# Performance work log

Hardware: AMD Instinct MI355X
Metric: run time of the kernel (lower is better)

Reference implementation:

```python
import jax, jax.numpy as jnp
import numpy as np

B = 256          # batch
H = 1024         # conditioning_size (dec_hid_dim)
D = 256          # gst_dim
G = 32           # num_gst
C = 16           # num_cells
O = 256          # output_size


def setup_inputs() -> dict:
    key = jax.random.key(0)
    ks = jax.random.split(key, 7)
    hidden = jax.random.normal(ks[0], (B, H), dtype=jnp.float32)
    # per-cell embedding tables: nn.Embedding(num_gst, gst_dim) stacked over cells
    gst_emb = jax.random.normal(ks[1], (C, G, D), dtype=jnp.float32)
    # per-cell Linear(gst_dim + cond, cond): weight [H, H + D] (torch [out, in]), bias [H]
    attn_w = jax.random.normal(ks[2], (C, H, H + D), dtype=jnp.float32) * 0.02
    attn_b = jax.random.normal(ks[3], (C, H), dtype=jnp.float32) * 0.02
    # per-cell v: Parameter(torch.rand(cond))
    v = jax.random.uniform(ks[4], (C, H), dtype=jnp.float32)
    # out Linear(gst_dim, output_size)
    out_w = jax.random.normal(ks[5], (O, D), dtype=jnp.float32) * 0.02
    out_b = jax.random.normal(ks[6], (O,), dtype=jnp.float32) * 0.02
    return {"hidden": hidden, "gst_emb": gst_emb, "attn_w": attn_w,
            "attn_b": attn_b, "v": v, "out_w": out_w, "out_b": out_b}


def reference(hidden, gst_emb, attn_w, attn_b, v, out_w, out_b):
    # Original concatenates (hidden, encoder_outputs) along features; split the
    # linear weight accordingly instead of materializing the concat.
    w_hid = attn_w[:, :, :H]        # [C, H, H]
    w_enc = attn_w[:, :, H:]        # [C, H, D]
    # embedding lookup of arange(G) == the table rows themselves (same for all batch)
    enc = gst_emb                   # [C, G, D]
    hid_part = jnp.einsum('bh,coh->bco', hidden, w_hid)     # [B, C, Ho]
    enc_part = jnp.einsum('cgd,cod->cgo', enc, w_enc)       # [C, G, Ho]
    energy = jnp.tanh(hid_part[:, :, None, :] + enc_part[None]
                      + attn_b[None, :, None, :])           # [B, C, G, Ho]
    scores = jnp.einsum('bcgh,ch->bcg', energy, v)          # [B, C, G]
    attention = jax.nn.softmax(scores, axis=-1)             # softmax over num_gst
    weighted = jnp.einsum('bcg,cgd->bcd', attention, enc)   # [B, C, D]
    att_cat = attention.reshape(B, C * G)                   # torch.cat(att_list, dim=1)
    pooled = jnp.mean(weighted, axis=1)                     # [B, D]
    out = pooled @ out_w.T + out_b                          # [B, O]
    return (att_cat, out)
```

## Files before the change

### kernel.cpp

```cpp
#include <hip/hip_runtime.h>
#include <hip/hip_bf16.h>

#define B_  256
#define H_  1024
#define D_  256
#define G_  32
#define C_  16
#define O_  256
#define HD_ 1280
#define N1_ 16384
#define RS_ 36

typedef __attribute__((ext_vector_type(8))) short short8;
typedef __attribute__((ext_vector_type(4))) short s16x4;
typedef __attribute__((ext_vector_type(4))) float f32x4;

#define MFMA16(a, b, c) __builtin_amdgcn_mfma_f32_16x16x32_bf16((a), (b), (c), 0, 0, 0)

__device__ __forceinline__ float tanh_c(float x) {
    float y = __expf(2.f * x);
    float t = 1.f - 2.f * __builtin_amdgcn_rcpf(y + 1.f);
    return fminf(fmaxf(t, -0.99999994f), 0.99999994f);
}

__device__ __forceinline__ short bfhi(float x) {
    return (short)(__float_as_uint(x) >> 16);
}
__device__ __forceinline__ short bflo(float x) {
    float fhi = __uint_as_float(__float_as_uint(x) & 0xFFFF0000u);
    return (short)(__float_as_uint(x - fhi) >> 16);
}

__device__ __forceinline__ void split4(const float4 v, s16x4& hi, s16x4& lo) {
    hi[0] = bfhi(v.x); lo[0] = bflo(v.x);
    hi[1] = bfhi(v.y); lo[1] = bflo(v.y);
    hi[2] = bfhi(v.z); lo[2] = bflo(v.z);
    hi[3] = bfhi(v.w); lo[3] = bflo(v.w);
}

__global__ __launch_bounds__(256) void gemm12_kernel(
    const float* __restrict__ hidden, const float* __restrict__ enc,
    const float* __restrict__ attn_w, const float* __restrict__ attn_b,
    float* __restrict__ hp, float* __restrict__ ep)
{
    __shared__ short AsH[64 * RS_];
    __shared__ short AsL[64 * RS_];
    __shared__ short BsH[64 * RS_];
    __shared__ short BsL[64 * RS_];

    const int tid  = threadIdx.x;
    const int wave = tid >> 6, lane = tid & 63;
    const int l16 = lane & 15;
    const int lk  = (lane >> 4) * 8;

    if (blockIdx.x < 4) {
        const int m0 = blockIdx.x * 64;
        const int n0 = blockIdx.y * 64;
        const int wm = (wave >> 1) * 32;
        const int wn = (wave & 1) * 32;

        f32x4 acc[2][2];
        #pragma unroll
        for (int mi = 0; mi < 2; ++mi)
            #pragma unroll
            for (int ni = 0; ni < 2; ++ni)
                acc[mi][ni] = f32x4{0.f, 0.f, 0.f, 0.f};

        const int r0 = tid >> 3;
        const int c0 = (tid & 7) * 4;
        const float* pA = hidden + (size_t)(m0 + r0) * H_ + c0;
        const float* pB = attn_w + (size_t)(n0 + r0) * HD_ + c0;
        const int dA = 32 * H_;
        const int dB = 32 * HD_;

        float4 a0[2], a1[2], b0[2], b1[2];
        a0[0] = *(const float4*)(pA);
        a1[0] = *(const float4*)(pA + dA);
        b0[0] = *(const float4*)(pB);
        b1[0] = *(const float4*)(pB + dB);
        a0[1] = *(const float4*)(pA + 32);
        a1[1] = *(const float4*)(pA + dA + 32);
        b0[1] = *(const float4*)(pB + 32);
        b1[1] = *(const float4*)(pB + dB + 32);

#define G1_BODY(S, K0)                                                        \
        {                                                                     \
            __builtin_amdgcn_s_barrier();                                     \
            { s16x4 h_, l_; split4(a0[S], h_, l_);                            \
              *(s16x4*)(AsH + r0 * RS_ + c0) = h_;                            \
              *(s16x4*)(AsL + r0 * RS_ + c0) = l_; }                          \
            { s16x4 h_, l_; split4(a1[S], h_, l_);                            \
              *(s16x4*)(AsH + (r0 + 32) * RS_ + c0) = h_;                     \
              *(s16x4*)(AsL + (r0 + 32) * RS_ + c0) = l_; }                   \
            { s16x4 h_, l_; split4(b0[S], h_, l_);                            \
              *(s16x4*)(BsH + r0 * RS_ + c0) = h_;                            \
              *(s16x4*)(BsL + r0 * RS_ + c0) = l_; }                          \
            { s16x4 h_, l_; split4(b1[S], h_, l_);                            \
              *(s16x4*)(BsH + (r0 + 32) * RS_ + c0) = h_;                     \
              *(s16x4*)(BsL + (r0 + 32) * RS_ + c0) = l_; }                   \
            asm volatile("s_waitcnt lgkmcnt(0)" ::: "memory");                \
            __builtin_amdgcn_s_barrier();                                     \
            if ((K0) + 64 < H_) {                                             \
                a0[S] = *(const float4*)(pA + (K0) + 64);                     \
                a1[S] = *(const float4*)(pA + dA + (K0) + 64);                \
                b0[S] = *(const float4*)(pB + (K0) + 64);                     \
                b1[S] = *(const float4*)(pB + dB + (K0) + 64);                \
            }                                                                 \
            short8 ah_[2], al_[2], bh_[2], bl_[2];                            \
            _Pragma("unroll")                                                 \
            for (int mi = 0; mi < 2; ++mi) {                                  \
                ah_[mi] = *(const short8*)(AsH + (wm + mi * 16 + l16) * RS_ + lk); \
                al_[mi] = *(const short8*)(AsL + (wm + mi * 16 + l16) * RS_ + lk); \
            }                                                                 \
            _Pragma("unroll")                                                 \
            for (int ni = 0; ni < 2; ++ni) {                                  \
                bh_[ni] = *(const short8*)(BsH + (wn + ni * 16 + l16) * RS_ + lk); \
                bl_[ni] = *(const short8*)(BsL + (wn + ni * 16 + l16) * RS_ + lk); \
            }                                                                 \
            _Pragma("unroll")                                                 \
            for (int mi = 0; mi < 2; ++mi)                                    \
                _Pragma("unroll")                                             \
                for (int ni = 0; ni < 2; ++ni) {                              \
                    acc[mi][ni] = MFMA16(ah_[mi], bh_[ni], acc[mi][ni]);      \
                    acc[mi][ni] = MFMA16(al_[mi], bh_[ni], acc[mi][ni]);      \
                    acc[mi][ni] = MFMA16(ah_[mi], bl_[ni], acc[mi][ni]);      \
                }                                                             \
        }

        for (int k0 = 0; k0 < H_; k0 += 64) {
            G1_BODY(0, k0)
            G1_BODY(1, k0 + 32)
        }
#undef G1_BODY

        const int lr = (lane >> 4) * 4;
        #pragma unroll
        for (int mi = 0; mi < 2; ++mi) {
            #pragma unroll
            for (int ni = 0; ni < 2; ++ni) {
                const int col   = n0 + wn + ni * 16 + l16;
                const float bias = attn_b[col];
                float* dst = hp + (size_t)(m0 + wm + mi * 16 + lr) * N1_ + col;
                f32x4 vacc = acc[mi][ni];
                dst[0]       = tanh_c(vacc[0] + bias);
                dst[N1_]     = tanh_c(vacc[1] + bias);
                dst[2 * N1_] = tanh_c(vacc[2] + bias);
                dst[3 * N1_] = tanh_c(vacc[3] + bias);
            }
        }
    } else {
        const int c  = blockIdx.y & 15;
        const int n0 = (blockIdx.y >> 4) * 64 + wave * 16;

        f32x4 acc[2];
        acc[0] = f32x4{0.f, 0.f, 0.f, 0.f};
        acc[1] = f32x4{0.f, 0.f, 0.f, 0.f};

        const float* encp = enc + c * (G_ * D_);
        const float* wp   = attn_w + (size_t)c * H_ * HD_ + H_;

        #pragma unroll
        for (int kk = 0; kk < 8; ++kk) {
            const int k0 = kk * 32 + lk;
            short8 ah[2], al[2], bh, bl;
            #pragma unroll
            for (int mi = 0; mi < 2; ++mi) {
                const float* p = encp + (mi * 16 + l16) * D_ + k0;
                s16x4 h0, l0, h1, l1;
                split4(*(const float4*)p, h0, l0);
                split4(*(const float4*)(p + 4), h1, l1);
                ah[mi] = short8{h0[0],h0[1],h0[2],h0[3],h1[0],h1[1],h1[2],h1[3]};
                al[mi] = short8{l0[0],l0[1],l0[2],l0[3],l1[0],l1[1],l1[2],l1[3]};
            }
            {
                const float* p = wp + (size_t)(n0 + l16) * HD_ + k0;
                s16x4 h0, l0, h1, l1;
                split4(*(const float4*)p, h0, l0);
                split4(*(const float4*)(p + 4), h1, l1);
                bh = short8{h0[0],h0[1],h0[2],h0[3],h1[0],h1[1],h1[2],h1[3]};
                bl = short8{l0[0],l0[1],l0[2],l0[3],l1[0],l1[1],l1[2],l1[3]};
            }
            #pragma unroll
            for (int mi = 0; mi < 2; ++mi) {
                acc[mi] = MFMA16(ah[mi], bh, acc[mi]);
                acc[mi] = MFMA16(al[mi], bh, acc[mi]);
                acc[mi] = MFMA16(ah[mi], bl, acc[mi]);
            }
        }

        const int lr = (lane >> 4) * 4;
        #pragma unroll
        for (int mi = 0; mi < 2; ++mi) {
            const int g = mi * 16 + lr;
            const int o = n0 + l16;
            float* dst = ep + (c * G_ + g) * H_ + o;
            f32x4 vacc = acc[mi];
            dst[0]      = tanh_c(vacc[0]);
            dst[H_]     = tanh_c(vacc[1]);
            dst[2 * H_] = tanh_c(vacc[2]);
            dst[3 * H_] = tanh_c(vacc[3]);
        }
    }
}

__global__ __launch_bounds__(256) void attn_kernel(
    const float* __restrict__ hp, const float* __restrict__ ep,
    const float* __restrict__ v, const float* __restrict__ enc,
    float* __restrict__ out, float* __restrict__ wt)
{
    const int c  = blockIdx.x;
    const int b0 = blockIdx.y * 4;
    const int tid  = threadIdx.x;
    const int wave = tid >> 6, lane = tid & 63;

    __shared__ float s_att[4][G_];
    __shared__ float s_sc[4][G_];

    f32x4 vv[4], tav[4][4];
    const float* vrow = v + c * H_;
    #pragma unroll
    for (int j = 0; j < 4; ++j)
        vv[j] = *(const f32x4*)(vrow + lane * 4 + j * 256);
    #pragma unroll
    for (int bi = 0; bi < 4; ++bi) {
        const float* hprow = hp + (size_t)(b0 + bi) * N1_ + c * H_;
        #pragma unroll
        for (int j = 0; j < 4; ++j)
            tav[bi][j] = *(const f32x4*)(hprow + lane * 4 + j * 256);
    }

    #pragma unroll
    for (int gg = 0; gg < 8; ++gg) {
        const int g = wave * 8 + gg;
        const float* eprow = ep + (size_t)(c * G_ + g) * H_;
        float s[4] = {0.f, 0.f, 0.f, 0.f};
        #pragma unroll
        for (int j = 0; j < 4; ++j) {
            const f32x4 tb = *(const f32x4*)(eprow + lane * 4 + j * 256);
            #pragma unroll
            for (int e = 0; e < 4; ++e) {
                const float tbx = tb[e];
                const float w   = vv[j][e];
                #pragma unroll
                for (int bi = 0; bi < 4; ++bi) {
                    const float ta  = tav[bi][j][e];
                    const float num = ta + tbx;
                    const float den = fmaf(ta, tbx, 1.f);
                    s[bi] = fmaf(num * __builtin_amdgcn_rcpf(den), w, s[bi]);
                }
            }
        }
        #pragma unroll
        for (int off = 32; off > 0; off >>= 1) {
            s[0] += __shfl_down(s[0], off, 64);
            s[1] += __shfl_down(s[1], off, 64);
            s[2] += __shfl_down(s[2], off, 64);
            s[3] += __shfl_down(s[3], off, 64);
        }
        if (lane == 0) {
            s_sc[0][g] = s[0]; s_sc[1][g] = s[1];
            s_sc[2][g] = s[2]; s_sc[3][g] = s[3];
        }
    }
    __syncthreads();

    if (tid < 128) {
        const int bi = tid >> 5, g = tid & 31;
        float sv = s_sc[bi][g];
        float m = sv;
        #pragma unroll
        for (int off = 16; off > 0; off >>= 1)
            m = fmaxf(m, __shfl_xor(m, off, 32));
        const float e = __expf(sv - m);
        float sum = e;
        #pragma unroll
        for (int off = 16; off > 0; off >>= 1)
            sum += __shfl_xor(sum, off, 32);
        const float a = e / sum;
        s_att[bi][g] = a;
        out[(size_t)(b0 + bi) * (C_ * G_) + c * G_ + g] = a;
    }
    __syncthreads();

    float w0 = 0.f, w1 = 0.f, w2 = 0.f, w3 = 0.f;
    const float* encc = enc + c * (G_ * D_) + tid;
    #pragma unroll
    for (int g = 0; g < G_; ++g) {
        const float e = encc[g * D_];
        w0 = fmaf(s_att[0][g], e, w0);
        w1 = fmaf(s_att[1][g], e, w1);
        w2 = fmaf(s_att[2][g], e, w2);
        w3 = fmaf(s_att[3][g], e, w3);
    }
    wt[(size_t)((b0 + 0) * C_ + c) * D_ + tid] = w0;
    wt[(size_t)((b0 + 1) * C_ + c) * D_ + tid] = w1;
    wt[(size_t)((b0 + 2) * C_ + c) * D_ + tid] = w2;
    wt[(size_t)((b0 + 3) * C_ + c) * D_ + tid] = w3;
}

__global__ __launch_bounds__(256) void out_kernel(
    const float* __restrict__ wt, const float* __restrict__ out_w,
    const float* __restrict__ out_b, float* __restrict__ out)
{
    const int b = blockIdx.x, tid = threadIdx.x;
    __shared__ float pooled[D_];

    float s = 0.f;
    #pragma unroll
    for (int c = 0; c < C_; ++c)
        s += wt[(size_t)(b * C_ + c) * D_ + tid];
    pooled[tid] = s * (1.f / 16.f);
    __syncthreads();

    float acc = out_b[tid];
    const float* wrow = out_w + tid * D_;
    #pragma unroll 8
    for (int dc = 0; dc < 64; ++dc) {
        float4 w4 = *(const float4*)(wrow + dc * 4);
        acc += pooled[dc * 4 + 0] * w4.x;
        acc += pooled[dc * 4 + 1] * w4.y;
        acc += pooled[dc * 4 + 2] * w4.z;
        acc += pooled[dc * 4 + 3] * w4.w;
    }
    out[(size_t)B_ * (C_ * G_) + b * O_ + tid] = acc;
}

extern "C" void kernel_launch(void* const* d_in, const int* in_sizes, int n_in,
                              void* d_out, int out_size, void* d_ws, size_t ws_size,
                              hipStream_t stream) {
    const float* hidden = (const float*)d_in[0];
    const float* enc    = (const float*)d_in[1];
    const float* attn_w = (const float*)d_in[2];
    const float* attn_b = (const float*)d_in[3];
    const float* v      = (const float*)d_in[4];
    const float* out_w  = (const float*)d_in[5];
    const float* out_b  = (const float*)d_in[6];
    float* out = (float*)d_out;

    float* hp = (float*)d_ws;
    float* ep = hp + (size_t)B_ * N1_;
    float* wt = ep + (size_t)C_ * G_ * H_;

    gemm12_kernel<<<dim3(5, 256), 256, 0, stream>>>(hidden, enc, attn_w, attn_b, hp, ep);
    attn_kernel<<<dim3(C_, B_ / 4), 256, 0, stream>>>(hp, ep, v, enc, out, wt);
    out_kernel<<<B_, 256, 0, stream>>>(wt, out_w, out_b, out);
}
```

Before: 220.4 us.

## Split GEMMs, pre-split hidden to bf16 pairs, use 32x32 MFMA with double-buffered LDS

The fused gemm12 kernel is split in two. The enc-projection kernel now also converts `hidden` into bf16 hi/lo arrays once, so the hidden-projection kernel no longer re-splits A tiles on every block. The hidden GEMM moves to 128x64 tiles using 32x32x16 MFMA, double-buffered LDS with one barrier per slab, and a padded stride of 40. This reduces redundant conversion work and barriers per k-step, at the cost of an extra launch, extra workspace traffic for hidH/hidL, and fewer blocks (512) along M.

```diff
diff --git a/kernel.cpp b/kernel.cpp
--- a/kernel.cpp
+++ b/kernel.cpp
@@ -9,13 +9,14 @@
 #define O_  256
 #define HD_ 1280
 #define N1_ 16384
-#define RS_ 36
-
-typedef __attribute__((ext_vector_type(8))) short short8;
-typedef __attribute__((ext_vector_type(4))) short s16x4;
-typedef __attribute__((ext_vector_type(4))) float f32x4;
-
-#define MFMA16(a, b, c) __builtin_amdgcn_mfma_f32_16x16x32_bf16((a), (b), (c), 0, 0, 0)
+#define RS_ 40
+
+typedef __attribute__((ext_vector_type(8)))  short short8;
+typedef __attribute__((ext_vector_type(4)))  short s16x4;
+typedef __attribute__((ext_vector_type(4)))  float f32x4;
+typedef __attribute__((ext_vector_type(16))) float f32x16;
+
+#define MFMA32(a, b, c) __builtin_amdgcn_mfma_f32_32x32x16_bf16((a), (b), (c), 0, 0, 0)
 
 __device__ __forceinline__ float tanh_c(float x) {
     float y = __expf(2.f * x);
@@ -38,169 +39,209 @@
     hi[3] = bfhi(v.w); lo[3] = bflo(v.w);
 }
 
-__global__ __launch_bounds__(256) void gemm12_kernel(
-    const float* __restrict__ hidden, const float* __restrict__ enc,
+__global__ __launch_bounds__(256, 2) void gemm1_kernel(
+    const short* __restrict__ hidH, const short* __restrict__ hidL,
     const float* __restrict__ attn_w, const float* __restrict__ attn_b,
-    float* __restrict__ hp, float* __restrict__ ep)
+    float* __restrict__ hp)
 {
-    __shared__ short AsH[64 * RS_];
-    __shared__ short AsL[64 * RS_];
-    __shared__ short BsH[64 * RS_];
-    __shared__ short BsL[64 * RS_];
+    __shared__ short AsH[2][128 * RS_];
+    __shared__ short AsL[2][128 * RS_];
+    __shared__ short BsH[2][64 * RS_];
+    __shared__ short BsL[2][64 * RS_];
 
     const int tid  = threadIdx.x;
     const int wave = tid >> 6, lane = tid & 63;
+    const int m0 = blockIdx.x * 128;
+    const int n0 = blockIdx.y * 64;
+    const int wm = (wave >> 1) * 64;
+    const int wn = (wave & 1) * 32;
+    const int l31 = lane & 31;
+    const int kh  = (lane >> 5) * 8;
+
+    f32x16 acc0, acc1;
+    #pragma unroll
+    for (int i = 0; i < 16; ++i) { acc0[i] = 0.f; acc1[i] = 0.f; }
+
+    const int rA = tid >> 2, cA = (tid & 3) * 8;
+    const int rB = tid >> 3, cB = (tid & 7) * 4;
+    const short* pAH0 = hidH + (size_t)(m0 + rA) * H_ + cA;
+    const short* pAH1 = pAH0 + 64 * H_;
+    const short* pAL0 = hidL + (size_t)(m0 + rA) * H_ + cA;
+    const short* pAL1 = pAL0 + 64 * H_;
+    const float* pB0  = attn_w + (size_t)(n0 + rB) * HD_ + cB;
+    const float* pB1  = pB0 + (size_t)32 * HD_;
+
+    const int wA0 = rA * RS_ + cA, wA1 = wA0 + 64 * RS_;
+    const int wB0 = rB * RS_ + cB, wB1 = wB0 + 32 * RS_;
+    const int aoff0 = (wm + l31) * RS_ + kh;
+    const int aoff1 = aoff0 + 32 * RS_;
+    const int boff  = (wn + l31) * RS_ + kh;
+
+    short8 raH[2][2], raL[2][2];
+    float4 rb[2][2];
+
+    raH[0][0] = *(const short8*)(pAH0);       raH[0][1] = *(const short8*)(pAH1);
+    raL[0][0] = *(const short8*)(pAL0);       raL[0][1] = *(const short8*)(pAL1);
+    rb[0][0]  = *(const float4*)(pB0);        rb[0][1]  = *(const float4*)(pB1);
+    raH[1][0] = *(const short8*)(pAH0 + 32);  raH[1][1] = *(const short8*)(pAH1 + 32);
+    raL[1][0] = *(const short8*)(pAL0 + 32);  raL[1][1] = *(const short8*)(pAL1 + 32);
+    rb[1][0]  = *(const float4*)(pB0 + 32);   rb[1][1]  = *(const float4*)(pB1 + 32);
+
+    *(short8*)(&AsH[0][wA0]) = raH[0][0];
+    *(short8*)(&AsH[0][wA1]) = raH[0][1];
+    *(short8*)(&AsL[0][wA0]) = raL[0][0];
+    *(short8*)(&AsL[0][wA1]) = raL[0][1];
+    {   s16x4 h_, l_;
+        split4(rb[0][0], h_, l_);
+        *(s16x4*)(&BsH[0][wB0]) = h_; *(s16x4*)(&BsL[0][wB0]) = l_;
+        split4(rb[0][1], h_, l_);
+        *(s16x4*)(&BsH[0][wB1]) = h_; *(s16x4*)(&BsL[0][wB1]) = l_;
+    }
+    raH[0][0] = *(const short8*)(pAH0 + 64);  raH[0][1] = *(const short8*)(pAH1 + 64);
+    raL[0][0] = *(const short8*)(pAL0 + 64);  raL[0][1] = *(const short8*)(pAL1 + 64);
+    rb[0][0]  = *(const float4*)(pB0 + 64);   rb[0][1]  = *(const float4*)(pB1 + 64);
+
+    asm volatile("s_waitcnt lgkmcnt(0)" ::: "memory");
+    __builtin_amdgcn_s_barrier();
+
+#define SLAB(P, DOW, DOL, KL, DOB)                                            \
+    {                                                                         \
+        if (DOW) {                                                            \
+            *(short8*)(&AsH[P ^ 1][wA0]) = raH[P ^ 1][0];                     \
+            *(short8*)(&AsH[P ^ 1][wA1]) = raH[P ^ 1][1];                     \
+            *(short8*)(&AsL[P ^ 1][wA0]) = raL[P ^ 1][0];                     \
+            *(short8*)(&AsL[P ^ 1][wA1]) = raL[P ^ 1][1];                     \
+            s16x4 h_, l_;                                                     \
+            split4(rb[P ^ 1][0], h_, l_);                                     \
+            *(s16x4*)(&BsH[P ^ 1][wB0]) = h_;                                 \
+            *(s16x4*)(&BsL[P ^ 1][wB0]) = l_;                                 \
+            split4(rb[P ^ 1][1], h_, l_);                                     \
+            *(s16x4*)(&BsH[P ^ 1][wB1]) = h_;                                 \
+            *(s16x4*)(&BsL[P ^ 1][wB1]) = l_;                                 \
+        }                                                                     \
+        if (DOL) {                                                            \
+            raH[P ^ 1][0] = *(const short8*)(pAH0 + (KL));                    \
+            raH[P ^ 1][1] = *(const short8*)(pAH1 + (KL));                    \
+            raL[P ^ 1][0] = *(const short8*)(pAL0 + (KL));                    \
+            raL[P ^ 1][1] = *(const short8*)(pAL1 + (KL));                    \
+            rb[P ^ 1][0]  = *(const float4*)(pB0 + (KL));                     \
+            rb[P ^ 1][1]  = *(const float4*)(pB1 + (KL));                     \
+        }                                                                     \
+        _Pragma("unroll")                                                     \
+        for (int ks = 0; ks < 2; ++ks) {                                      \
+            short8 ah0 = *(const short8*)(&AsH[P][aoff0 + ks * 16]);          \
+            short8 ah1 = *(const short8*)(&AsH[P][aoff1 + ks * 16]);          \
+            short8 al0 = *(const short8*)(&AsL[P][aoff0 + ks * 16]);          \
+            short8 al1 = *(const short8*)(&AsL[P][aoff1 + ks * 16]);          \
+            short8 bh  = *(const short8*)(&BsH[P][boff + ks * 16]);           \
+            short8 bl  = *(const short8*)(&BsL[P][boff + ks * 16]);           \
+            acc0 = MFMA32(ah0, bh, acc0);                                     \
+            acc1 = MFMA32(ah1, bh, acc1);                                     \
+            acc0 = MFMA32(al0, bh, acc0);                                     \
+            acc1 = MFMA32(al1, bh, acc1);                                     \
+            acc0 = MFMA32(ah0, bl, acc0);                                     \
+            acc1 = MFMA32(ah1, bl, acc1);                                     \
+        }                                                                     \
+        if (DOB) {                                                            \
+            asm volatile("s_waitcnt lgkmcnt(0)" ::: "memory");                \
+            __builtin_amdgcn_s_barrier();                                     \
+        }                                                                     \
+    }
+
+    for (int S = 0; S < 28; S += 2) {
+        SLAB(0, 1, 1, (S + 3) * 32, 1)
+        SLAB(1, 1, 1, (S + 4) * 32, 1)
+    }
+    SLAB(0, 1, 1, 31 * 32, 1)
+    SLAB(1, 1, 0, 0, 1)
+    SLAB(0, 1, 0, 0, 1)
+    SLAB(1, 0, 0, 0, 0)
+#undef SLAB
+
+    const int col  = n0 + wn + l31;
+    const float bias = attn_b[col];
+    const int rbase = m0 + wm + (lane >> 5) * 4;
+    float* dcol = hp + col;
+    #pragma unroll
+    for (int r = 0; r < 16; ++r) {
+        const int row = rbase + (r & 3) + 8 * (r >> 2);
+        dcol[(size_t)row * N1_]        = tanh_c(acc0[r] + bias);
+        dcol[(size_t)(row + 32) * N1_] = tanh_c(acc1[r] + bias);
+    }
+}
+
+__global__ __launch_bounds__(256) void gemm2_kernel(
+    const float* __restrict__ enc, const float* __restrict__ attn_w,
+    const float* __restrict__ hidden, float* __restrict__ ep,
+    short* __restrict__ hidH, short* __restrict__ hidL)
+{
+    const int tid  = threadIdx.x;
+    const int wave = tid >> 6, lane = tid & 63;
+
+    {
+        const int base = (blockIdx.y * 16 + blockIdx.x) * 1024 + tid * 4;
+        const float4 h4 = *(const float4*)(hidden + base);
+        s16x4 hh, ll;
+        split4(h4, hh, ll);
+        *(s16x4*)(hidH + base) = hh;
+        *(s16x4*)(hidL + base) = ll;
+    }
+
+    const int c  = blockIdx.y;
+    const int n0 = blockIdx.x * 64 + wave * 16;
     const int l16 = lane & 15;
     const int lk  = (lane >> 4) * 8;
 
-    if (blockIdx.x < 4) {
-        const int m0 = blockIdx.x * 64;
-        const int n0 = blockIdx.y * 64;
-        const int wm = (wave >> 1) * 32;
-        const int wn = (wave & 1) * 32;
-
-        f32x4 acc[2][2];
-        #pragma unroll
-        for (int mi = 0; mi < 2; ++mi)
-            #pragma unroll
-            for (int ni = 0; ni < 2; ++ni)
-                acc[mi][ni] = f32x4{0.f, 0.f, 0.f, 0.f};
-
-        const int r0 = tid >> 3;
-        const int c0 = (tid & 7) * 4;
-        const float* pA = hidden + (size_t)(m0 + r0) * H_ + c0;
-        const float* pB = attn_w + (size_t)(n0 + r0) * HD_ + c0;
-        const int dA = 32 * H_;
-        const int dB = 32 * HD_;
-
-        float4 a0[2], a1[2], b0[2], b1[2];
-        a0[0] = *(const float4*)(pA);
-        a1[0] = *(const float4*)(pA + dA);
-        b0[0] = *(const float4*)(pB);
-        b1[0] = *(const float4*)(pB + dB);
-        a0[1] = *(const float4*)(pA + 32);
-        a1[1] = *(const float4*)(pA + dA + 32);
-        b0[1] = *(const float4*)(pB + 32);
-        b1[1] = *(const float4*)(pB + dB + 32);
-
-#define G1_BODY(S, K0)                                                        \
-        {                                                                     \
-            __builtin_amdgcn_s_barrier();                                     \
-            { s16x4 h_, l_; split4(a0[S], h_, l_);                            \
-              *(s16x4*)(AsH + r0 * RS_ + c0) = h_;                            \
-              *(s16x4*)(AsL + r0 * RS_ + c0) = l_; }                          \
-            { s16x4 h_, l_; split4(a1[S], h_, l_);                            \
-              *(s16x4*)(AsH + (r0 + 32) * RS_ + c0) = h_;                     \
-              *(s16x4*)(AsL + (r0 + 32) * RS_ + c0) = l_; }                   \
-            { s16x4 h_, l_; split4(b0[S], h_, l_);                            \
-              *(s16x4*)(BsH + r0 * RS_ + c0) = h_;                            \
-              *(s16x4*)(BsL + r0 * RS_ + c0) = l_; }                          \
-            { s16x4 h_, l_; split4(b1[S], h_, l_);                            \
-              *(s16x4*)(BsH + (r0 + 32) * RS_ + c0) = h_;                     \
-              *(s16x4*)(BsL + (r0 + 32) * RS_ + c0) = l_; }                   \
-            asm volatile("s_waitcnt lgkmcnt(0)" ::: "memory");                \
-            __builtin_amdgcn_s_barrier();                                     \
-            if ((K0) + 64 < H_) {                                             \
-                a0[S] = *(const float4*)(pA + (K0) + 64);                     \
-                a1[S] = *(const float4*)(pA + dA + (K0) + 64);                \
-                b0[S] = *(const float4*)(pB + (K0) + 64);                     \
-                b1[S] = *(const float4*)(pB + dB + (K0) + 64);                \
-            }                                                                 \
-            short8 ah_[2], al_[2], bh_[2], bl_[2];                            \
-            _Pragma("unroll")                                                 \
-            for (int mi = 0; mi < 2; ++mi) {                                  \
-                ah_[mi] = *(const short8*)(AsH + (wm + mi * 16 + l16) * RS_ + lk); \
-                al_[mi] = *(const short8*)(AsL + (wm + mi * 16 + l16) * RS_ + lk); \
-            }                                                                 \
-            _Pragma("unroll")                                                 \
-            for (int ni = 0; ni < 2; ++ni) {                                  \
-                bh_[ni] = *(const short8*)(BsH + (wn + ni * 16 + l16) * RS_ + lk); \
-                bl_[ni] = *(const short8*)(BsL + (wn + ni * 16 + l16) * RS_ + lk); \
-            }                                                                 \
-            _Pragma("unroll")                                                 \
-            for (int mi = 0; mi < 2; ++mi)                                    \
-                _Pragma("unroll")                                             \
-                for (int ni = 0; ni < 2; ++ni) {                              \
-                    acc[mi][ni] = MFMA16(ah_[mi], bh_[ni], acc[mi][ni]);      \
-                    acc[mi][ni] = MFMA16(al_[mi], bh_[ni], acc[mi][ni]);      \
-                    acc[mi][ni] = MFMA16(ah_[mi], bl_[ni], acc[mi][ni]);      \
-                }                                                             \
-        }
-
-        for (int k0 = 0; k0 < H_; k0 += 64) {
-            G1_BODY(0, k0)
-            G1_BODY(1, k0 + 32)
-        }
-#undef G1_BODY
-
-        const int lr = (lane >> 4) * 4;
+#define MFMA16(a, b, c) __builtin_amdgcn_mfma_f32_16x16x32_bf16((a), (b), (c), 0, 0, 0)
+    f32x4 acc[2];
+    acc[0] = f32x4{0.f, 0.f, 0.f, 0.f};
+    acc[1] = f32x4{0.f, 0.f, 0.f, 0.f};
+
+    const float* encp = enc + c * (G_ * D_);
+    const float* wp   = attn_w + (size_t)c * H_ * HD_ + H_;
+
+    #pragma unroll
+    for (int kk = 0; kk < 8; ++kk) {
+        const int k0 = kk * 32 + lk;
+        short8 ah[2], al[2], bh, bl;
         #pragma unroll
         for (int mi = 0; mi < 2; ++mi) {
-            #pragma unroll
-            for (int ni = 0; ni < 2; ++ni) {
-                const int col   = n0 + wn + ni * 16 + l16;
-                const float bias = attn_b[col];
-                float* dst = hp + (size_t)(m0 + wm + mi * 16 + lr) * N1_ + col;
-                f32x4 vacc = acc[mi][ni];
-                dst[0]       = tanh_c(vacc[0] + bias);
-                dst[N1_]     = tanh_c(vacc[1] + bias);
-                dst[2 * N1_] = tanh_c(vacc[2] + bias);
-                dst[3 * N1_] = tanh_c(vacc[3] + bias);
-            }
-        }
-    } else {
-        const int c  = blockIdx.y & 15;
-        const int n0 = (blockIdx.y >> 4) * 64 + wave * 16;
-
-        f32x4 acc[2];
-        acc[0] = f32x4{0.f, 0.f, 0.f, 0.f};
-        acc[1] = f32x4{0.f, 0.f, 0.f, 0.f};
-
-        const float* encp = enc + c * (G_ * D_);
-        const float* wp   = attn_w + (size_t)c * H_ * HD_ + H_;
-
-        #pragma unroll
-        for (int kk = 0; kk < 8; ++kk) {
-            const int k0 = kk * 32 + lk;
-            short8 ah[2], al[2], bh, bl;
-            #pragma unroll
-            for (int mi = 0; mi < 2; ++mi) {
-                const float* p = encp + (mi * 16 + l16) * D_ + k0;
-                s16x4 h0, l0, h1, l1;
-                split4(*(const float4*)p, h0, l0);
-                split4(*(const float4*)(p + 4), h1, l1);
-                ah[mi] = short8{h0[0],h0[1],h0[2],h0[3],h1[0],h1[1],h1[2],h1[3]};
-                al[mi] = short8{l0[0],l0[1],l0[2],l0[3],l1[0],l1[1],l1[2],l1[3]};
-            }
-            {
-                const float* p = wp + (size_t)(n0 + l16) * HD_ + k0;
-                s16x4 h0, l0, h1, l1;
-                split4(*(const float4*)p, h0, l0);
-                split4(*(const float4*)(p + 4), h1, l1);
-                bh = short8{h0[0],h0[1],h0[2],h0[3],h1[0],h1[1],h1[2],h1[3]};
-                bl = short8{l0[0],l0[1],l0[2],l0[3],l1[0],l1[1],l1[2],l1[3]};
-            }
-            #pragma unroll
-            for (int mi = 0; mi < 2; ++mi) {
-                acc[mi] = MFMA16(ah[mi], bh, acc[mi]);
-                acc[mi] = MFMA16(al[mi], bh, acc[mi]);
-                acc[mi] = MFMA16(ah[mi], bl, acc[mi]);
-            }
-        }
-
-        const int lr = (lane >> 4) * 4;
+            const float* p = encp + (mi * 16 + l16) * D_ + k0;
+            s16x4 h0, l0, h1, l1;
+            split4(*(const float4*)p, h0, l0);
+            split4(*(const float4*)(p + 4), h1, l1);
+            ah[mi] = short8{h0[0],h0[1],h0[2],h0[3],h1[0],h1[1],h1[2],h1[3]};
+            al[mi] = short8{l0[0],l0[1],l0[2],l0[3],l1[0],l1[1],l1[2],l1[3]};
+        }
+        {
+            const float* p = wp + (size_t)(n0 + l16) * HD_ + k0;
+            s16x4 h0, l0, h1, l1;
+            split4(*(const float4*)p, h0, l0);
+            split4(*(const float4*)(p + 4), h1, l1);
+            bh = short8{h0[0],h0[1],h0[2],h0[3],h1[0],h1[1],h1[2],h1[3]};
+            bl = short8{l0[0],l0[1],l0[2],l0[3],l1[0],l1[1],l1[2],l1[3]};
+        }
         #pragma unroll
         for (int mi = 0; mi < 2; ++mi) {
-            const int g = mi * 16 + lr;
-            const int o = n0 + l16;
-            float* dst = ep + (c * G_ + g) * H_ + o;
-            f32x4 vacc = acc[mi];
-            dst[0]      = tanh_c(vacc[0]);
-            dst[H_]     = tanh_c(vacc[1]);
-            dst[2 * H_] = tanh_c(vacc[2]);
-            dst[3 * H_] = tanh_c(vacc[3]);
-        }
-    }
+            acc[mi] = MFMA16(ah[mi], bh, acc[mi]);
+            acc[mi] = MFMA16(al[mi], bh, acc[mi]);
+            acc[mi] = MFMA16(ah[mi], bl, acc[mi]);
+        }
+    }
+
+    const int lr = (lane >> 4) * 4;
+    #pragma unroll
+    for (int mi = 0; mi < 2; ++mi) {
+        const int g = mi * 16 + lr;
+        const int o = n0 + l16;
+        float* dst = ep + (c * G_ + g) * H_ + o;
+        f32x4 vacc = acc[mi];
+        dst[0]      = tanh_c(vacc[0]);
+        dst[H_]     = tanh_c(vacc[1]);
+        dst[2 * H_] = tanh_c(vacc[2]);
+        dst[3 * H_] = tanh_c(vacc[3]);
+    }
+#undef MFMA16
 }
 
 __global__ __launch_bounds__(256) void attn_kernel(
@@ -340,8 +381,11 @@
     float* hp = (float*)d_ws;
     float* ep = hp + (size_t)B_ * N1_;
     float* wt = ep + (size_t)C_ * G_ * H_;
-
-    gemm12_kernel<<<dim3(5, 256), 256, 0, stream>>>(hidden, enc, attn_w, attn_b, hp, ep);
+    short* hidH = (short*)(wt + (size_t)B_ * C_ * D_);
+    short* hidL = hidH + (size_t)B_ * H_;
+
+    gemm2_kernel<<<dim3(16, C_), 256, 0, stream>>>(enc, attn_w, hidden, ep, hidH, hidL);
+    gemm1_kernel<<<dim3(2, 256), 256, 0, stream>>>(hidH, hidL, attn_w, attn_b, hp);
     attn_kernel<<<dim3(C_, B_ / 4), 256, 0, stream>>>(hp, ep, v, enc, out, wt);
     out_kernel<<<B_, 256, 0, stream>>>(wt, out_w, out_b, out);
 }
```

Result: faster. 213.3 us (-3.2%).
